# Kernel optimization log

Hardware: AMD Instinct MI355X
Metric: run time of the kernel (lower is better)

The kernel has to match this reference:

```python
import jax, jax.numpy as jnp
import numpy as np

N_NODES = 100_000
N_EDGES = 1_600_000
N_GRAPHS = 256
IN_DIM, HID, HEADS, LAYERS = 480, 128, 4, 3
HEAD_DIM = HID // HEADS
NEG_SLOPE = 0.2
LN_EPS = 1e-5


def setup_inputs() -> dict:
    key = jax.random.key(0)
    ks = jax.random.split(key, 12)
    x = jax.random.normal(ks[0], (N_NODES, IN_DIM), dtype=jnp.float32)
    edge_index = jax.random.randint(ks[1], (2, N_EDGES), 0, N_NODES, dtype=jnp.int32)
    batch = jnp.sort(jax.random.randint(ks[2], (N_NODES,), 0, N_GRAPHS, dtype=jnp.int32))
    s_in = 1.0 / np.sqrt(IN_DIM)
    s_h = 1.0 / np.sqrt(HID)
    return {
        "x": x,
        "W_in": jax.random.uniform(ks[3], (IN_DIM, HID), jnp.float32, -s_in, s_in),
        "b_in": jax.random.uniform(ks[4], (HID,), jnp.float32, -s_in, s_in),
        "W_gat": jax.random.uniform(ks[5], (LAYERS, HID, HID), jnp.float32, -s_h, s_h),
        "att_src": jax.random.uniform(ks[6], (LAYERS, HEADS, HEAD_DIM), jnp.float32, -s_h, s_h),
        "att_dst": jax.random.uniform(ks[7], (LAYERS, HEADS, HEAD_DIM), jnp.float32, -s_h, s_h),
        "b_gat": jnp.zeros((LAYERS, HID), jnp.float32),
        "ln_g": jnp.ones((LAYERS, HID), jnp.float32),
        "ln_b": jnp.zeros((LAYERS, HID), jnp.float32),
        "edge_index": edge_index,
        "batch": batch,
    }


def _gat_conv(h_in, W, a_src, a_dst, bias, src, dst, n):
    # h: [N, H, D] per-head projected features
    h = (h_in @ W).reshape(n, HEADS, HEAD_DIM)
    asrc = jnp.sum(h * a_src, axis=-1)  # [N, H]
    adst = jnp.sum(h * a_dst, axis=-1)  # [N, H]
    e = jax.nn.leaky_relu(asrc[src] + adst[dst], NEG_SLOPE)  # [E, H]
    # scatter-softmax over incoming edges of each destination node
    emax = jax.ops.segment_max(e, dst, num_segments=n)  # [N, H]
    emax = jnp.where(jnp.isfinite(emax), emax, 0.0)
    ex = jnp.exp(e - emax[dst])
    denom = jax.ops.segment_sum(ex, dst, num_segments=n)
    alpha = ex / jnp.maximum(denom, 1e-16)[dst]  # [E, H]
    out = jax.ops.segment_sum(alpha[:, :, None] * h[src], dst, num_segments=n)
    return out.reshape(n, HID) + bias


def _layer_norm(x, g, b):
    mu = jnp.mean(x, axis=-1, keepdims=True)
    var = jnp.mean(jnp.square(x - mu), axis=-1, keepdims=True)
    return (x - mu) * jax.lax.rsqrt(var + LN_EPS) * g + b


def reference(x, W_in, b_in, W_gat, att_src, att_dst, b_gat, ln_g, ln_b, edge_index, batch):
    n = x.shape[0]
    # PyG GATConv default add_self_loops=True
    loop = jnp.arange(n, dtype=edge_index.dtype)
    src = jnp.concatenate([edge_index[0], loop])
    dst = jnp.concatenate([edge_index[1], loop])

    h = jax.nn.relu(x @ W_in + b_in)
    for l in range(LAYERS):
        residual = h
        h = _gat_conv(h, W_gat[l], att_src[l], att_dst[l], b_gat[l], src, dst, n)
        h = jax.nn.relu(_layer_norm(h, ln_g[l], ln_b[l]))
        # dropout omitted (eval mode)
        h = h + residual
    # global mean pool per graph
    sums = jax.ops.segment_sum(h, batch, num_segments=N_GRAPHS)
    cnt = jax.ops.segment_sum(jnp.ones((n,), h.dtype), batch, num_segments=N_GRAPHS)
    return sums / jnp.maximum(cnt, 1.0)[:, None]
```

## Files before the change

### kernel.cpp

```cpp
#include <hip/hip_runtime.h>
#include <hip/hip_bf16.h>

#define HID 128
#define NEG_SLOPE 0.2f
#define LN_EPS 1e-5f
#define SEG_CAP 8192

typedef __attribute__((ext_vector_type(8))) short short8;
typedef __attribute__((ext_vector_type(4))) float floatx4;

__device__ __forceinline__ float us2f(unsigned short u) {
    union { unsigned int i; float f; } c; c.i = ((unsigned int)u) << 16; return c.f;
}
__device__ __forceinline__ float lo2f(unsigned u) {
    union { unsigned int i; float f; } c; c.i = u << 16; return c.f;
}
__device__ __forceinline__ float hi2f(unsigned u) {
    union { unsigned int i; float f; } c; c.i = u & 0xffff0000u; return c.f;
}
__device__ __forceinline__ unsigned short f2us(float f) {
    union { float f; unsigned u; } c; c.f = f;
    unsigned r = c.u + 0x7FFF + ((c.u >> 16) & 1);
    return (unsigned short)(r >> 16);
}
__device__ __forceinline__ unsigned pack2(float a, float b) {
    return (unsigned)f2us(a) | ((unsigned)f2us(b) << 16);
}
__device__ __forceinline__ float ldw(const void* p, long i, int bf) {
    return bf ? us2f(((const unsigned short*)p)[i]) : ((const float*)p)[i];
}
__device__ __forceinline__ float lrelu(float x) { return x > 0.f ? x : NEG_SLOPE * x; }
__device__ __forceinline__ float wsum(float x) {
#pragma unroll
    for (int o = 32; o > 0; o >>= 1) x += __shfl_xor(x, o);
    return x;
}
__device__ __forceinline__ float wmaxr(float x) {
#pragma unroll
    for (int o = 32; o > 0; o >>= 1) x = fmaxf(x, __shfl_xor(x, o));
    return x;
}
__device__ __forceinline__ float pick4(float4 v, int h) {
    return h == 0 ? v.x : (h == 1 ? v.y : (h == 2 ? v.z : v.w));
}

__global__ void detect_kernel(const float* __restrict__ x, int* __restrict__ flag) {
    float v = x[threadIdx.x];
    int bad = (!(v == v)) || (fabsf(v) > 1e6f);
    unsigned long long m = __ballot(bad);
    if (threadIdx.x == 0) flag[0] = (m != 0ull) ? 1 : 0;
}

__global__ __launch_bounds__(256) void zero_int_kernel(int* p, int n) {
    int i = blockIdx.x * 256 + threadIdx.x;
    if (i < n) p[i] = 0;
}

__global__ __launch_bounds__(256) void bucket_hist_kernel(const int* __restrict__ dst, int E, int nb,
                                                          int* __restrict__ bucket_cnt) {
    __shared__ int hist[512];
    for (int i = threadIdx.x; i < nb; i += 256) hist[i] = 0;
    __syncthreads();
    const int base = blockIdx.x * 4096;
    const int end = min(base + 4096, E);
    for (int i = base + threadIdx.x; i < end; i += 256)
        atomicAdd(&hist[dst[i] >> 8], 1);
    __syncthreads();
    for (int i = threadIdx.x; i < nb; i += 256)
        if (hist[i]) atomicAdd(&bucket_cnt[i], hist[i]);
}

__global__ __launch_bounds__(512) void bucket_scan_kernel(const int* __restrict__ bucket_cnt,
                                                          int* __restrict__ bucket_base,
                                                          int* __restrict__ cursor,
                                                          int nb, int* __restrict__ row_ptr, int N) {
    __shared__ int sc[512];
    const int t = threadIdx.x;
    const int v = (t < nb) ? bucket_cnt[t] : 0;
    int x = v;
    sc[t] = x;
    __syncthreads();
    for (int o = 1; o < 512; o <<= 1) {
        const int y = (t >= o) ? sc[t - o] : 0;
        __syncthreads();
        x += y;
        sc[t] = x;
        __syncthreads();
    }
    if (t < nb) { bucket_base[t] = x - v; cursor[t] = x - v; }
    if (t == nb - 1) { bucket_base[nb] = x; row_ptr[N] = x; }
}

__global__ __launch_bounds__(256) void partition_kernel(const int* __restrict__ src, const int* __restrict__ dst,
                                                        int E, int nb, int* __restrict__ cursor,
                                                        unsigned long long* __restrict__ tmp) {
    __shared__ int hist[512];
    __shared__ int tbase[512];
    for (int i = threadIdx.x; i < nb; i += 256) hist[i] = 0;
    __syncthreads();
    const int base = blockIdx.x * 4096;
    const int end = min(base + 4096, E);
    int myd[16], mys[16], myr[16];
#pragma unroll
    for (int j = 0; j < 16; ++j) {
        const int i = base + threadIdx.x + j * 256;
        if (i < end) {
            const int d = dst[i];
            myd[j] = d;
            mys[j] = src[i];
            myr[j] = atomicAdd(&hist[d >> 8], 1);
        } else {
            myd[j] = -1;
        }
    }
    __syncthreads();
    for (int i = threadIdx.x; i < nb; i += 256) {
        const int hv = hist[i];
        tbase[i] = hv ? atomicAdd(&cursor[i], hv) : 0;
    }
    __syncthreads();
#pragma unroll
    for (int j = 0; j < 16; ++j) {
        if (myd[j] >= 0) {
            const int b = myd[j] >> 8;
            tmp[(size_t)tbase[b] + myr[j]] = ((unsigned long long)(unsigned)myd[j] << 32) | (unsigned)mys[j];
        }
    }
}

__global__ __launch_bounds__(256) void bucket_sort_kernel(const unsigned long long* __restrict__ tmp,
                                                          const int* __restrict__ bucket_base,
                                                          int* __restrict__ row_ptr, int* __restrict__ csr,
                                                          int N) {
    __shared__ int hist[256];
    __shared__ int sc[256];
    __shared__ int off[256];
    __shared__ int outb[SEG_CAP];
    const int b = blockIdx.x;
    const int node0 = b << 8;
    const int nn = min(256, N - node0);
    const int s0 = bucket_base[b], s1 = bucket_base[b + 1];
    const int cnt = s1 - s0;
    const int t = threadIdx.x;
    hist[t] = 0;
    __syncthreads();
    for (int i = s0 + t; i < s1; i += 256) {
        const int d = (int)(tmp[i] >> 32) - node0;
        atomicAdd(&hist[d], 1);
    }
    __syncthreads();
    const int v = hist[t];
    int x = v;
    sc[t] = x;
    __syncthreads();
    for (int o = 1; o < 256; o <<= 1) {
        const int y = (t >= o) ? sc[t - o] : 0;
        __syncthreads();
        x += y;
        sc[t] = x;
        __syncthreads();
    }
    off[t] = x - v;
    if (t < nn) row_ptr[node0 + t] = s0 + (x - v);
    hist[t] = 0;
    __syncthreads();
    if (cnt <= SEG_CAP) {
        for (int i = s0 + t; i < s1; i += 256) {
            const unsigned long long pr = tmp[i];
            const int d = (int)(pr >> 32) - node0;
            const int p = off[d] + atomicAdd(&hist[d], 1);
            outb[p] = (int)(unsigned)(pr & 0xffffffffu);
        }
        __syncthreads();
        for (int i = t; i < cnt; i += 256) csr[s0 + i] = outb[i];
    } else {
        for (int i = s0 + t; i < s1; i += 256) {
            const unsigned long long pr = tmp[i];
            const int d = (int)(pr >> 32) - node0;
            const int p = off[d] + atomicAdd(&hist[d], 1);
            csr[s0 + p] = (int)(unsigned)(pr & 0xffffffffu);
        }
    }
}

__global__ __launch_bounds__(256) void transpose_w_kernel(const void* __restrict__ W, long w_off, int K,
                                                          unsigned short* __restrict__ Wt,
                                                          const int* __restrict__ flagp) {
    const int bf = flagp[0];
    const int i = blockIdx.x * 256 + threadIdx.x;
    if (i >= 128 * K) return;
    const int n = i / K, k = i - n * K;
    const long s = w_off + (long)k * 128 + n;
    Wt[i] = bf ? ((const unsigned short*)W)[s] : f2us(((const float*)W)[s]);
}

template <int C_BF>
__global__ __launch_bounds__(256) void mfma_gemm_kernel(const void* __restrict__ Ap, int a_input,
                                                        const unsigned short* __restrict__ Bt,
                                                        const void* __restrict__ bias, long bias_off,
                                                        void* __restrict__ Cp,
                                                        int M, int K, int do_relu,
                                                        const int* __restrict__ flagp) {
    __shared__ unsigned short As[128 * 40];
    __shared__ unsigned short Bs[128 * 40];
    const int bf = flagp[0];
    const int a_bf = a_input ? bf : 2;
    const int t = threadIdx.x;
    const int bm = blockIdx.x * 128;
    const int lane = t & 63, wave = t >> 6;
    const int r = lane & 15, quad = lane >> 4;
    const int srow = t >> 1, skh = (t & 1) * 16;

    floatx4 acc[2][8];
#pragma unroll
    for (int mt = 0; mt < 2; ++mt)
#pragma unroll
        for (int nt = 0; nt < 8; ++nt)
#pragma unroll
            for (int q = 0; q < 4; ++q) acc[mt][nt][q] = 0.f;

    for (int k0 = 0; k0 < K; k0 += 32) {
        {
            const int grow = bm + srow;
            uint4 u0 = make_uint4(0, 0, 0, 0), u1 = u0;
            if (grow < M) {
                const long aidx = (long)grow * K + k0 + skh;
                if (a_bf == 1) {
                    const unsigned short* ap = (const unsigned short*)Ap + aidx;
                    u0 = ((const uint4*)ap)[0];
                    u1 = ((const uint4*)ap)[1];
                } else {
                    const float* ap = (const float*)Ap + aidx;
                    float4 f0 = ((const float4*)ap)[0];
                    float4 f1 = ((const float4*)ap)[1];
                    float4 f2 = ((const float4*)ap)[2];
                    float4 f3 = ((const float4*)ap)[3];
                    u0 = make_uint4(pack2(f0.x, f0.y), pack2(f0.z, f0.w), pack2(f1.x, f1.y), pack2(f1.z, f1.w));
                    u1 = make_uint4(pack2(f2.x, f2.y), pack2(f2.z, f2.w), pack2(f3.x, f3.y), pack2(f3.z, f3.w));
                }
            }
            *(uint4*)&As[srow * 40 + skh]     = u0;
            *(uint4*)&As[srow * 40 + skh + 8] = u1;
        }
        {
            const unsigned short* bp = Bt + (long)srow * K + k0 + skh;
            uint4 v0 = ((const uint4*)bp)[0];
            uint4 v1 = ((const uint4*)bp)[1];
            *(uint4*)&Bs[srow * 40 + skh]     = v0;
            *(uint4*)&Bs[srow * 40 + skh + 8] = v1;
        }
        __syncthreads();

        short8 afr[2];
        afr[0] = *(const short8*)&As[(wave * 32 + r) * 40 + quad * 8];
        afr[1] = *(const short8*)&As[(wave * 32 + 16 + r) * 40 + quad * 8];
#pragma unroll
        for (int nt = 0; nt < 8; ++nt) {
            short8 bfr = *(const short8*)&Bs[(nt * 16 + r) * 40 + quad * 8];
            acc[0][nt] = __builtin_amdgcn_mfma_f32_16x16x32_bf16(afr[0], bfr, acc[0][nt], 0, 0, 0);
            acc[1][nt] = __builtin_amdgcn_mfma_f32_16x16x32_bf16(afr[1], bfr, acc[1][nt], 0, 0, 0);
        }
        __syncthreads();
    }

    float bb[8];
#pragma unroll
    for (int nt = 0; nt < 8; ++nt) bb[nt] = bias ? ldw(bias, bias_off + nt * 16 + r, bf) : 0.f;

#pragma unroll
    for (int mt = 0; mt < 2; ++mt) {
        const int gr0 = bm + wave * 32 + mt * 16 + quad * 4;
#pragma unroll
        for (int reg = 0; reg < 4; ++reg) {
            const int grow = gr0 + reg;
            if (grow < M) {
#pragma unroll
                for (int nt = 0; nt < 8; ++nt) {
                    float v = acc[mt][nt][reg] + bb[nt];
                    if (do_relu) v = fmaxf(v, 0.f);
                    const long ci = (long)grow * HID + nt * 16 + r;
                    if (C_BF) ((unsigned short*)Cp)[ci] = f2us(v);
                    else      ((float*)Cp)[ci] = v;
                }
            }
        }
    }
}

__global__ __launch_bounds__(256) void attn_kernel(const unsigned short* __restrict__ hp,
                                                   const void* __restrict__ att_src,
                                                   const void* __restrict__ att_dst, long a_off,
                                                   float* __restrict__ asrc, float* __restrict__ adst,
                                                   int N, const int* __restrict__ flagp) {
    __shared__ float sA[128], sD[128];
    const int bf = flagp[0];
    const int t = threadIdx.x;
    if (t < 128) { sA[t] = ldw(att_src, a_off + t, bf); sD[t] = ldw(att_dst, a_off + t, bf); }
    __syncthreads();
    const int gid = blockIdx.x * 256 + t;
    if (gid >= N * 4) return;
    const int n = gid >> 2, hd = gid & 3;
    const unsigned short* p = hp + (size_t)n * HID + hd * 32;
    float s1 = 0.f, s2 = 0.f;
#pragma unroll
    for (int q = 0; q < 4; ++q) {
        uint4 v = ((const uint4*)p)[q];
        unsigned arr[4] = {v.x, v.y, v.z, v.w};
#pragma unroll
        for (int j = 0; j < 4; ++j) {
            const int k = q * 8 + j * 2;
            float lo = lo2f(arr[j]);
            float hi = hi2f(arr[j]);
            s1 += lo * sA[hd * 32 + k] + hi * sA[hd * 32 + k + 1];
            s2 += lo * sD[hd * 32 + k] + hi * sD[hd * 32 + k + 1];
        }
    }
    asrc[gid] = s1;
    adst[gid] = s2;
}

__global__ __launch_bounds__(256) void gat_kernel(float* __restrict__ h,
                                                  const unsigned short* __restrict__ hp,
                                                  const float* __restrict__ asrc,
                                                  const float* __restrict__ adst,
                                                  const int* __restrict__ row_ptr,
                                                  const int* __restrict__ csr,
                                                  const void* __restrict__ bgat,
                                                  const void* __restrict__ lng,
                                                  const void* __restrict__ lnb, long w_off,
                                                  int N, const int* __restrict__ flagp) {
    __shared__ uint2 ebuf[4][320];
    const int bf = flagp[0];
    const int lane = threadIdx.x & 63;
    const int wslot = threadIdx.x >> 6;
    const int head = lane >> 4;
    const int n = (blockIdx.x << 2) | wslot;
    if (n >= N) return;

    const int e0 = row_ptr[n], e1 = row_ptr[n + 1];
    const int d = e1 - e0;
    const float4 ad4 = *(const float4*)(adst + (size_t)n * 4);
    const float4 as4 = *(const float4*)(asrc + (size_t)n * 4);
    float4 es;
    es.x = lrelu(as4.x + ad4.x); es.y = lrelu(as4.y + ad4.y);
    es.z = lrelu(as4.z + ad4.z); es.w = lrelu(as4.w + ad4.w);

    float2 acc;
    float4 dn, exs;
    const int l2 = lane * 2;

    if (d <= 64) {
        int s = 0;
        float4 l4 = es;
        if (lane < d) {
            s = csr[e0 + lane];
            const float4 a = *(const float4*)(asrc + (size_t)s * 4);
            l4.x = lrelu(a.x + ad4.x);
            l4.y = lrelu(a.y + ad4.y);
            l4.z = lrelu(a.z + ad4.z);
            l4.w = lrelu(a.w + ad4.w);
        }
        float4 m;
        m.x = fmaxf(wmaxr(l4.x), es.x);
        m.y = fmaxf(wmaxr(l4.y), es.y);
        m.z = fmaxf(wmaxr(l4.z), es.z);
        m.w = fmaxf(wmaxr(l4.w), es.w);

        exs.x = expf(es.x - m.x); exs.y = expf(es.y - m.y);
        exs.z = expf(es.z - m.z); exs.w = expf(es.w - m.w);

        float4 ex4 = make_float4(0.f, 0.f, 0.f, 0.f);
        if (lane < d) {
            ex4.x = expf(l4.x - m.x);
            ex4.y = expf(l4.y - m.y);
            ex4.z = expf(l4.z - m.z);
            ex4.w = expf(l4.w - m.w);
        }
        dn.x = wsum(ex4.x) + exs.x;
        dn.y = wsum(ex4.y) + exs.y;
        dn.z = wsum(ex4.z) + exs.z;
        dn.w = wsum(ex4.w) + exs.w;

        uint2* eb = ebuf[wslot];
        const unsigned su = (unsigned)s;
        eb[lane * 5 + 0] = make_uint2(su, __float_as_uint(ex4.x));
        eb[lane * 5 + 1] = make_uint2(su, __float_as_uint(ex4.y));
        eb[lane * 5 + 2] = make_uint2(su, __float_as_uint(ex4.z));
        eb[lane * 5 + 3] = make_uint2(su, __float_as_uint(ex4.w));

        const float wself = pick4(exs, head);
        const unsigned hv0 = *(const unsigned*)(hp + (size_t)n * HID + l2);
        acc.x = wself * lo2f(hv0);
        acc.y = wself * hi2f(hv0);

        float2 a0 = {0.f, 0.f}, a1 = {0.f, 0.f}, a2 = {0.f, 0.f}, a3 = {0.f, 0.f};
        int i = 0;
        for (; i + 4 <= d; i += 4) {
            const uint2 q0 = eb[(i + 0) * 5 + head];
            const uint2 q1 = eb[(i + 1) * 5 + head];
            const uint2 q2 = eb[(i + 2) * 5 + head];
            const uint2 q3 = eb[(i + 3) * 5 + head];
            const unsigned u0 = *(const unsigned*)(hp + (size_t)q0.x * HID + l2);
            const unsigned u1 = *(const unsigned*)(hp + (size_t)q1.x * HID + l2);
            const unsigned u2 = *(const unsigned*)(hp + (size_t)q2.x * HID + l2);
            const unsigned u3 = *(const unsigned*)(hp + (size_t)q3.x * HID + l2);
            const float w0 = __uint_as_float(q0.y);
            const float w1 = __uint_as_float(q1.y);
            const float w2 = __uint_as_float(q2.y);
            const float w3 = __uint_as_float(q3.y);
            a0.x = fmaf(w0, lo2f(u0), a0.x); a0.y = fmaf(w0, hi2f(u0), a0.y);
            a1.x = fmaf(w1, lo2f(u1), a1.x); a1.y = fmaf(w1, hi2f(u1), a1.y);
            a2.x = fmaf(w2, lo2f(u2), a2.x); a2.y = fmaf(w2, hi2f(u2), a2.y);
            a3.x = fmaf(w3, lo2f(u3), a3.x); a3.y = fmaf(w3, hi2f(u3), a3.y);
        }
        for (; i < d; ++i) {
            const uint2 q = eb[i * 5 + head];
            const unsigned u = *(const unsigned*)(hp + (size_t)q.x * HID + l2);
            const float wq = __uint_as_float(q.y);
            acc.x = fmaf(wq, lo2f(u), acc.x);
            acc.y = fmaf(wq, hi2f(u), acc.y);
        }
        acc.x += (a0.x + a1.x) + (a2.x + a3.x);
        acc.y += (a0.y + a1.y) + (a2.y + a3.y);
    } else {
        float4 m = es;
        for (int e = e0 + lane; e < e1; e += 64) {
            const int s = csr[e];
            const float4 a = *(const float4*)(asrc + (size_t)s * 4);
            m.x = fmaxf(m.x, lrelu(a.x + ad4.x));
            m.y = fmaxf(m.y, lrelu(a.y + ad4.y));
            m.z = fmaxf(m.z, lrelu(a.z + ad4.z));
            m.w = fmaxf(m.w, lrelu(a.w + ad4.w));
        }
        m.x = wmaxr(m.x); m.y = wmaxr(m.y); m.z = wmaxr(m.z); m.w = wmaxr(m.w);

        exs.x = expf(es.x - m.x); exs.y = expf(es.y - m.y);
        exs.z = expf(es.z - m.z); exs.w = expf(es.w - m.w);

        const float wself = pick4(exs, head);
        const unsigned hv0 = *(const unsigned*)(hp + (size_t)n * HID + l2);
        acc.x = wself * lo2f(hv0);
        acc.y = wself * hi2f(hv0);
        dn = make_float4(0.f, 0.f, 0.f, 0.f);

        for (int base = e0; base < e1; base += 64) {
            const int cnt = min(64, e1 - base);
            int s = 0;
            float4 ex4 = make_float4(0.f, 0.f, 0.f, 0.f);
            if (base + lane < e1) {
                s = csr[base + lane];
                const float4 a = *(const float4*)(asrc + (size_t)s * 4);
                ex4.x = expf(lrelu(a.x + ad4.x) - m.x);
                ex4.y = expf(lrelu(a.y + ad4.y) - m.y);
                ex4.z = expf(lrelu(a.z + ad4.z) - m.z);
                ex4.w = expf(lrelu(a.w + ad4.w) - m.w);
                dn.x += ex4.x; dn.y += ex4.y; dn.z += ex4.z; dn.w += ex4.w;
            }
            for (int i = 0; i < cnt; ++i) {
                const int ss = __shfl(s, i);
                const float wx = __shfl(ex4.x, i);
                const float wy = __shfl(ex4.y, i);
                const float wz = __shfl(ex4.z, i);
                const float ww = __shfl(ex4.w, i);
                const float wgt = head == 0 ? wx : (head == 1 ? wy : (head == 2 ? wz : ww));
                const unsigned uv = *(const unsigned*)(hp + (size_t)ss * HID + l2);
                acc.x = fmaf(wgt, lo2f(uv), acc.x);
                acc.y = fmaf(wgt, hi2f(uv), acc.y);
            }
        }
        dn.x = wsum(dn.x) + exs.x;
        dn.y = wsum(dn.y) + exs.y;
        dn.z = wsum(dn.z) + exs.z;
        dn.w = wsum(dn.w) + exs.w;
    }

    const float invd = 1.f / fmaxf(pick4(dn, head), 1e-16f);
    acc.x *= invd; acc.y *= invd;
    acc.x += ldw(bgat, w_off + l2, bf);
    acc.y += ldw(bgat, w_off + l2 + 1, bf);

    float mean = wsum(acc.x + acc.y) * (1.f / 128.f);
    float dx = acc.x - mean, dy = acc.y - mean;
    float var = wsum(dx * dx + dy * dy) * (1.f / 128.f);
    float rstd = rsqrtf(var + LN_EPS);
    float o0 = dx * rstd * ldw(lng, w_off + l2, bf)     + ldw(lnb, w_off + l2, bf);
    float o1 = dy * rstd * ldw(lng, w_off + l2 + 1, bf) + ldw(lnb, w_off + l2 + 1, bf);
    o0 = fmaxf(o0, 0.f);
    o1 = fmaxf(o1, 0.f);

    const float2 r = *(const float2*)(h + (size_t)n * HID + l2);
    *(float2*)(h + (size_t)n * HID + l2) = make_float2(o0 + r.x, o1 + r.y);
}

__global__ __launch_bounds__(256) void pool_kernel(const float* __restrict__ h, const int* __restrict__ batch,
                                                   void* __restrict__ out, int N,
                                                   const int* __restrict__ flagp) {
    const int g = blockIdx.x;
    int a = 0, b = N;
    while (a < b) { int mid = (a + b) >> 1; if (batch[mid] < g) a = mid + 1; else b = mid; }
    const int lo = a;
    b = N;
    while (a < b) { int mid = (a + b) >> 1; if (batch[mid] <= g) a = mid + 1; else b = mid; }
    const int hi = a;

    const int col = threadIdx.x & 127;
    const int half = threadIdx.x >> 7;
    float s = 0.f;
    for (int r = lo + half; r < hi; r += 2) s += h[(size_t)r * HID + col];
    __shared__ float part[128];
    if (half == 0) part[col] = s;
    __syncthreads();
    if (half == 1) {
        const float tot = part[col] + s;
        const float v = tot / fmaxf((float)(hi - lo), 1.f);
        if (flagp[0]) ((unsigned short*)out)[g * HID + col] = f2us(v);
        else          ((float*)out)[g * HID + col] = v;
    }
}

extern "C" void kernel_launch(void* const* d_in, const int* in_sizes, int n_in,
                              void* d_out, int out_size, void* d_ws, size_t ws_size,
                              hipStream_t stream) {
    const void* x     = d_in[0];
    const void* W_in  = d_in[1];
    const void* b_in  = d_in[2];
    const void* W_gat = d_in[3];
    const void* att_s = d_in[4];
    const void* att_d = d_in[5];
    const void* b_gat = d_in[6];
    const void* ln_g  = d_in[7];
    const void* ln_b  = d_in[8];
    const int* edge_index = (const int*)d_in[9];
    const int* batch      = (const int*)d_in[10];

    const int N = in_sizes[10];
    const int E = in_sizes[9] / 2;
    const int IN_DIM = in_sizes[0] / N;
    const int n_graphs = out_size / HID;

    const int* esrc = edge_index;
    const int* edst = edge_index + E;

    char* w = (char*)d_ws;
    auto carve = [&](size_t bytes) -> void* {
        void* p = (void*)w;
        w += (bytes + 255) & ~(size_t)255;
        return p;
    };
    int* flag             = (int*)carve(256);
    int* row_ptr          = (int*)carve((size_t)(N + 1) * 4);
    int* csr              = (int*)carve((size_t)E * 4);
    float* asrc           = (float*)carve((size_t)N * 4 * 4);
    float* adst           = (float*)carve((size_t)N * 4 * 4);
    int* bucket_cnt       = (int*)carve(512 * 4);
    int* bucket_base      = (int*)carve(513 * 4);
    int* cursor           = (int*)carve(512 * 4);
    unsigned short* Wt_in = (unsigned short*)carve((size_t)HID * IN_DIM * 2);
    unsigned short* Wt_g  = (unsigned short*)carve((size_t)HID * HID * 2);
    float* h              = (float*)carve((size_t)N * HID * 4);
    unsigned short* hp    = (unsigned short*)carve((size_t)N * HID * 2);
    unsigned long long* tmp = (unsigned long long*)h;
    (void)ws_size; (void)n_in;

    detect_kernel<<<1, 64, 0, stream>>>((const float*)x, flag);

    const int nb = (N + 255) >> 8;
    const int ntiles = (E + 4095) / 4096;
    zero_int_kernel<<<2, 256, 0, stream>>>(bucket_cnt, 512);
    bucket_hist_kernel<<<ntiles, 256, 0, stream>>>(edst, E, nb, bucket_cnt);
    bucket_scan_kernel<<<1, 512, 0, stream>>>(bucket_cnt, bucket_base, cursor, nb, row_ptr, N);
    partition_kernel<<<ntiles, 256, 0, stream>>>(esrc, edst, E, nb, cursor, tmp);
    bucket_sort_kernel<<<nb, 256, 0, stream>>>(tmp, bucket_base, row_ptr, csr, N);

    transpose_w_kernel<<<(HID * IN_DIM + 255) / 256, 256, 0, stream>>>(W_in, 0, IN_DIM, Wt_in, flag);
    mfma_gemm_kernel<0><<<(N + 127) / 128, 256, 0, stream>>>(x, 1, Wt_in, b_in, 0, h, N, IN_DIM, 1, flag);

    for (int l = 0; l < 3; ++l) {
        transpose_w_kernel<<<(HID * HID + 255) / 256, 256, 0, stream>>>(W_gat, (long)l * HID * HID, HID, Wt_g, flag);
        mfma_gemm_kernel<1><<<(N + 127) / 128, 256, 0, stream>>>(h, 0, Wt_g, nullptr, 0, hp, N, HID, 0, flag);
        attn_kernel<<<(N * 4 + 255) / 256, 256, 0, stream>>>(hp, att_s, att_d, (long)l * HID,
                                                             asrc, adst, N, flag);
        gat_kernel<<<(N + 3) / 4, 256, 0, stream>>>(h, hp, asrc, adst, row_ptr, csr,
                                                    b_gat, ln_g, ln_b, (long)l * HID, N, flag);
    }

    pool_kernel<<<n_graphs, 256, 0, stream>>>(h, batch, d_out, N, flag);
}
```

Baseline: 831.4 us.

## Split GAT gather across half-waves and drop the softmax max pass

The GAT aggregation kernel is restructured so each half-wave processes alternate edges, with every lane loading four bf16 columns at once. The two half-wave partial sums are combined with a cross-half shuffle. The softmax no longer computes a per-destination max; it shifts by the self-loop score and uses fast __expf, which removes the wave max reductions and the separate max pass for high-degree nodes. The cost is some numeric-overflow risk if a neighbor score far exceeds the self score, plus duplicated LayerNorm work in both half-waves.

```diff
diff --git a/kernel.cpp b/kernel.cpp
--- a/kernel.cpp
+++ b/kernel.cpp
@@ -33,11 +33,6 @@
 __device__ __forceinline__ float wsum(float x) {
 #pragma unroll
     for (int o = 32; o > 0; o >>= 1) x += __shfl_xor(x, o);
-    return x;
-}
-__device__ __forceinline__ float wmaxr(float x) {
-#pragma unroll
-    for (int o = 32; o > 0; o >>= 1) x = fmaxf(x, __shfl_xor(x, o));
     return x;
 }
 __device__ __forceinline__ float pick4(float4 v, int h) {
@@ -333,163 +328,103 @@
     const int bf = flagp[0];
     const int lane = threadIdx.x & 63;
     const int wslot = threadIdx.x >> 6;
-    const int head = lane >> 4;
+    const int half = lane >> 5;
+    const int ll = lane & 31;
+    const int head4 = ll >> 3;
+    const int c0 = ll << 2;
     const int n = (blockIdx.x << 2) | wslot;
     if (n >= N) return;
 
     const int e0 = row_ptr[n], e1 = row_ptr[n + 1];
-    const int d = e1 - e0;
     const float4 ad4 = *(const float4*)(adst + (size_t)n * 4);
     const float4 as4 = *(const float4*)(asrc + (size_t)n * 4);
     float4 es;
     es.x = lrelu(as4.x + ad4.x); es.y = lrelu(as4.y + ad4.y);
     es.z = lrelu(as4.z + ad4.z); es.w = lrelu(as4.w + ad4.w);
 
-    float2 acc;
-    float4 dn, exs;
-    const int l2 = lane * 2;
-
-    if (d <= 64) {
+    const uint2 us = *(const uint2*)(hp + (size_t)n * HID + c0);
+    const float wself = half ? 0.f : 1.f;
+    float4 acc;
+    acc.x = wself * lo2f(us.x); acc.y = wself * hi2f(us.x);
+    acc.z = wself * lo2f(us.y); acc.w = wself * hi2f(us.y);
+
+    float4 dnp = make_float4(0.f, 0.f, 0.f, 0.f);
+    uint2* eb = ebuf[wslot];
+
+    for (int base = e0; base < e1; base += 64) {
+        const int cnt = min(64, e1 - base);
         int s = 0;
-        float4 l4 = es;
-        if (lane < d) {
-            s = csr[e0 + lane];
+        float4 ex4 = make_float4(0.f, 0.f, 0.f, 0.f);
+        if (lane < cnt) {
+            s = csr[base + lane];
             const float4 a = *(const float4*)(asrc + (size_t)s * 4);
-            l4.x = lrelu(a.x + ad4.x);
-            l4.y = lrelu(a.y + ad4.y);
-            l4.z = lrelu(a.z + ad4.z);
-            l4.w = lrelu(a.w + ad4.w);
-        }
-        float4 m;
-        m.x = fmaxf(wmaxr(l4.x), es.x);
-        m.y = fmaxf(wmaxr(l4.y), es.y);
-        m.z = fmaxf(wmaxr(l4.z), es.z);
-        m.w = fmaxf(wmaxr(l4.w), es.w);
-
-        exs.x = expf(es.x - m.x); exs.y = expf(es.y - m.y);
-        exs.z = expf(es.z - m.z); exs.w = expf(es.w - m.w);
-
-        float4 ex4 = make_float4(0.f, 0.f, 0.f, 0.f);
-        if (lane < d) {
-            ex4.x = expf(l4.x - m.x);
-            ex4.y = expf(l4.y - m.y);
-            ex4.z = expf(l4.z - m.z);
-            ex4.w = expf(l4.w - m.w);
-        }
-        dn.x = wsum(ex4.x) + exs.x;
-        dn.y = wsum(ex4.y) + exs.y;
-        dn.z = wsum(ex4.z) + exs.z;
-        dn.w = wsum(ex4.w) + exs.w;
-
-        uint2* eb = ebuf[wslot];
+            ex4.x = __expf(lrelu(a.x + ad4.x) - es.x);
+            ex4.y = __expf(lrelu(a.y + ad4.y) - es.y);
+            ex4.z = __expf(lrelu(a.z + ad4.z) - es.z);
+            ex4.w = __expf(lrelu(a.w + ad4.w) - es.w);
+            dnp.x += ex4.x; dnp.y += ex4.y; dnp.z += ex4.z; dnp.w += ex4.w;
+        }
         const unsigned su = (unsigned)s;
         eb[lane * 5 + 0] = make_uint2(su, __float_as_uint(ex4.x));
         eb[lane * 5 + 1] = make_uint2(su, __float_as_uint(ex4.y));
         eb[lane * 5 + 2] = make_uint2(su, __float_as_uint(ex4.z));
         eb[lane * 5 + 3] = make_uint2(su, __float_as_uint(ex4.w));
 
-        const float wself = pick4(exs, head);
-        const unsigned hv0 = *(const unsigned*)(hp + (size_t)n * HID + l2);
-        acc.x = wself * lo2f(hv0);
-        acc.y = wself * hi2f(hv0);
-
-        float2 a0 = {0.f, 0.f}, a1 = {0.f, 0.f}, a2 = {0.f, 0.f}, a3 = {0.f, 0.f};
-        int i = 0;
-        for (; i + 4 <= d; i += 4) {
-            const uint2 q0 = eb[(i + 0) * 5 + head];
-            const uint2 q1 = eb[(i + 1) * 5 + head];
-            const uint2 q2 = eb[(i + 2) * 5 + head];
-            const uint2 q3 = eb[(i + 3) * 5 + head];
-            const unsigned u0 = *(const unsigned*)(hp + (size_t)q0.x * HID + l2);
-            const unsigned u1 = *(const unsigned*)(hp + (size_t)q1.x * HID + l2);
-            const unsigned u2 = *(const unsigned*)(hp + (size_t)q2.x * HID + l2);
-            const unsigned u3 = *(const unsigned*)(hp + (size_t)q3.x * HID + l2);
-            const float w0 = __uint_as_float(q0.y);
-            const float w1 = __uint_as_float(q1.y);
-            const float w2 = __uint_as_float(q2.y);
-            const float w3 = __uint_as_float(q3.y);
-            a0.x = fmaf(w0, lo2f(u0), a0.x); a0.y = fmaf(w0, hi2f(u0), a0.y);
-            a1.x = fmaf(w1, lo2f(u1), a1.x); a1.y = fmaf(w1, hi2f(u1), a1.y);
-            a2.x = fmaf(w2, lo2f(u2), a2.x); a2.y = fmaf(w2, hi2f(u2), a2.y);
-            a3.x = fmaf(w3, lo2f(u3), a3.x); a3.y = fmaf(w3, hi2f(u3), a3.y);
-        }
-        for (; i < d; ++i) {
-            const uint2 q = eb[i * 5 + head];
-            const unsigned u = *(const unsigned*)(hp + (size_t)q.x * HID + l2);
-            const float wq = __uint_as_float(q.y);
-            acc.x = fmaf(wq, lo2f(u), acc.x);
-            acc.y = fmaf(wq, hi2f(u), acc.y);
-        }
-        acc.x += (a0.x + a1.x) + (a2.x + a3.x);
-        acc.y += (a0.y + a1.y) + (a2.y + a3.y);
-    } else {
-        float4 m = es;
-        for (int e = e0 + lane; e < e1; e += 64) {
-            const int s = csr[e];
-            const float4 a = *(const float4*)(asrc + (size_t)s * 4);
-            m.x = fmaxf(m.x, lrelu(a.x + ad4.x));
-            m.y = fmaxf(m.y, lrelu(a.y + ad4.y));
-            m.z = fmaxf(m.z, lrelu(a.z + ad4.z));
-            m.w = fmaxf(m.w, lrelu(a.w + ad4.w));
-        }
-        m.x = wmaxr(m.x); m.y = wmaxr(m.y); m.z = wmaxr(m.z); m.w = wmaxr(m.w);
-
-        exs.x = expf(es.x - m.x); exs.y = expf(es.y - m.y);
-        exs.z = expf(es.z - m.z); exs.w = expf(es.w - m.w);
-
-        const float wself = pick4(exs, head);
-        const unsigned hv0 = *(const unsigned*)(hp + (size_t)n * HID + l2);
-        acc.x = wself * lo2f(hv0);
-        acc.y = wself * hi2f(hv0);
-        dn = make_float4(0.f, 0.f, 0.f, 0.f);
-
-        for (int base = e0; base < e1; base += 64) {
-            const int cnt = min(64, e1 - base);
-            int s = 0;
-            float4 ex4 = make_float4(0.f, 0.f, 0.f, 0.f);
-            if (base + lane < e1) {
-                s = csr[base + lane];
-                const float4 a = *(const float4*)(asrc + (size_t)s * 4);
-                ex4.x = expf(lrelu(a.x + ad4.x) - m.x);
-                ex4.y = expf(lrelu(a.y + ad4.y) - m.y);
-                ex4.z = expf(lrelu(a.z + ad4.z) - m.z);
-                ex4.w = expf(lrelu(a.w + ad4.w) - m.w);
-                dn.x += ex4.x; dn.y += ex4.y; dn.z += ex4.z; dn.w += ex4.w;
-            }
-            for (int i = 0; i < cnt; ++i) {
-                const int ss = __shfl(s, i);
-                const float wx = __shfl(ex4.x, i);
-                const float wy = __shfl(ex4.y, i);
-                const float wz = __shfl(ex4.z, i);
-                const float ww = __shfl(ex4.w, i);
-                const float wgt = head == 0 ? wx : (head == 1 ? wy : (head == 2 ? wz : ww));
-                const unsigned uv = *(const unsigned*)(hp + (size_t)ss * HID + l2);
-                acc.x = fmaf(wgt, lo2f(uv), acc.x);
-                acc.y = fmaf(wgt, hi2f(uv), acc.y);
-            }
-        }
-        dn.x = wsum(dn.x) + exs.x;
-        dn.y = wsum(dn.y) + exs.y;
-        dn.z = wsum(dn.z) + exs.z;
-        dn.w = wsum(dn.w) + exs.w;
-    }
-
-    const float invd = 1.f / fmaxf(pick4(dn, head), 1e-16f);
-    acc.x *= invd; acc.y *= invd;
-    acc.x += ldw(bgat, w_off + l2, bf);
-    acc.y += ldw(bgat, w_off + l2 + 1, bf);
-
-    float mean = wsum(acc.x + acc.y) * (1.f / 128.f);
-    float dx = acc.x - mean, dy = acc.y - mean;
-    float var = wsum(dx * dx + dy * dy) * (1.f / 128.f);
-    float rstd = rsqrtf(var + LN_EPS);
-    float o0 = dx * rstd * ldw(lng, w_off + l2, bf)     + ldw(lnb, w_off + l2, bf);
-    float o1 = dy * rstd * ldw(lng, w_off + l2 + 1, bf) + ldw(lnb, w_off + l2 + 1, bf);
-    o0 = fmaxf(o0, 0.f);
-    o1 = fmaxf(o1, 0.f);
-
-    const float2 r = *(const float2*)(h + (size_t)n * HID + l2);
-    *(float2*)(h + (size_t)n * HID + l2) = make_float2(o0 + r.x, o1 + r.y);
+        float4 aA = make_float4(0.f, 0.f, 0.f, 0.f);
+        float4 aB = make_float4(0.f, 0.f, 0.f, 0.f);
+        int i = half;
+#define GAT_EDGE(idx, A)                                                      \
+        {                                                                     \
+            const uint2 q = eb[(idx) * 5 + head4];                            \
+            const uint2 u = *(const uint2*)(hp + (size_t)q.x * HID + c0);     \
+            const float wq = __uint_as_float(q.y);                            \
+            A.x = fmaf(wq, lo2f(u.x), A.x);                                   \
+            A.y = fmaf(wq, hi2f(u.x), A.y);                                   \
+            A.z = fmaf(wq, lo2f(u.y), A.z);                                   \
+            A.w = fmaf(wq, hi2f(u.y), A.w);                                   \
+        }
+        for (; i + 2 < cnt; i += 4) {
+            GAT_EDGE(i, aA);
+            GAT_EDGE(i + 2, aB);
+        }
+        for (; i < cnt; i += 2) GAT_EDGE(i, aA);
+#undef GAT_EDGE
+        acc.x += aA.x + aB.x; acc.y += aA.y + aB.y;
+        acc.z += aA.z + aB.z; acc.w += aA.w + aB.w;
+    }
+
+    acc.x += __shfl_xor(acc.x, 32);
+    acc.y += __shfl_xor(acc.y, 32);
+    acc.z += __shfl_xor(acc.z, 32);
+    acc.w += __shfl_xor(acc.w, 32);
+
+    float4 dn;
+    dn.x = wsum(dnp.x) + 1.f;
+    dn.y = wsum(dnp.y) + 1.f;
+    dn.z = wsum(dnp.z) + 1.f;
+    dn.w = wsum(dnp.w) + 1.f;
+
+    const float invd = 1.f / fmaxf(pick4(dn, head4), 1e-16f);
+    acc.x *= invd; acc.y *= invd; acc.z *= invd; acc.w *= invd;
+    acc.x += ldw(bgat, w_off + c0 + 0, bf);
+    acc.y += ldw(bgat, w_off + c0 + 1, bf);
+    acc.z += ldw(bgat, w_off + c0 + 2, bf);
+    acc.w += ldw(bgat, w_off + c0 + 3, bf);
+
+    const float mean = wsum(acc.x + acc.y + acc.z + acc.w) * (1.f / 256.f);
+    const float d0 = acc.x - mean, d1 = acc.y - mean, d2 = acc.z - mean, d3 = acc.w - mean;
+    const float var = wsum(d0 * d0 + d1 * d1 + d2 * d2 + d3 * d3) * (1.f / 256.f);
+    const float rstd = rsqrtf(var + LN_EPS);
+    float o0 = d0 * rstd * ldw(lng, w_off + c0 + 0, bf) + ldw(lnb, w_off + c0 + 0, bf);
+    float o1 = d1 * rstd * ldw(lng, w_off + c0 + 1, bf) + ldw(lnb, w_off + c0 + 1, bf);
+    float o2 = d2 * rstd * ldw(lng, w_off + c0 + 2, bf) + ldw(lnb, w_off + c0 + 2, bf);
+    float o3 = d3 * rstd * ldw(lng, w_off + c0 + 3, bf) + ldw(lnb, w_off + c0 + 3, bf);
+    o0 = fmaxf(o0, 0.f); o1 = fmaxf(o1, 0.f); o2 = fmaxf(o2, 0.f); o3 = fmaxf(o3, 0.f);
+
+    if (half == 0) {
+        const float4 r = *(const float4*)(h + (size_t)n * HID + c0);
+        *(float4*)(h + (size_t)n * HID + c0) = make_float4(o0 + r.x, o1 + r.y, o2 + r.z, o3 + r.w);
+    }
 }
 
 __global__ __launch_bounds__(256) void pool_kernel(const float* __restrict__ h, const int* __restrict__ batch,
```

New measurement: 900.9 us. 8.4% more time.
